# Performance work log

Measured on AMD Instinct MI355X. Metric: run time of the kernel, lower is better.

## Reference

```python
import jax, jax.numpy as jnp
import numpy as np

DIM = 2048
NH = 16
HD = 128
B = 32
BS = 16            # paged-KV block size
BLOCKS_PER_SEQ = 64
NUM_BLOCKS = B * BLOCKS_PER_SEQ
MAX_SEQ = BLOCKS_PER_SEQ * BS  # 1024
EPS = 1e-05


def _rms(x, w):
    return x * jax.lax.rsqrt(jnp.mean(x * x, axis=-1, keepdims=True) + EPS) * w


def setup_inputs() -> dict:
    key = jax.random.key(0)
    ks = jax.random.split(key, 12)
    init = lambda k, shape, fan: jax.random.normal(k, shape, jnp.float32) / np.float32(np.sqrt(fan))
    x = jax.random.normal(ks[0], (B, 1, DIM), jnp.float32)
    key_heap = jax.random.normal(ks[1], (NUM_BLOCKS, BS, NH, HD), jnp.float32)
    val_heap = jax.random.normal(ks[2], (NUM_BLOCKS, BS, NH, HD), jnp.float32)
    # each sequence owns a disjoint run of physical blocks
    block_table = jnp.arange(B * BLOCKS_PER_SEQ, dtype=jnp.int32).reshape(B, BLOCKS_PER_SEQ)
    context_lens = jax.random.randint(ks[3], (B,), 1, MAX_SEQ + 1, dtype=jnp.int32)
    last = context_lens - 1  # slot of the token being decoded
    blk = block_table[jnp.arange(B), last // BS]
    slot_mapping = (blk * BS + last % BS).astype(jnp.int32)
    return dict(
        x=x, key_heap=key_heap, val_heap=val_heap,
        wq=init(ks[4], (DIM, DIM), DIM), wk=init(ks[5], (DIM, DIM), DIM),
        wv=init(ks[6], (DIM, DIM), DIM), wo=init(ks[7], (DIM, DIM), DIM),
        w1=init(ks[8], (4 * DIM, DIM), DIM), w2=init(ks[9], (DIM, 4 * DIM), 4 * DIM),
        w3=init(ks[10], (4 * DIM, DIM), DIM),
        norm1_w=jnp.ones((DIM,), jnp.float32), norm2_w=jnp.ones((DIM,), jnp.float32),
        block_table=block_table, slot_mapping=slot_mapping,
        context_lens=context_lens, max_seq_len=MAX_SEQ,
    )


def reference(x, key_heap, val_heap, wq, wk, wv, wo, w1, w2, w3,
              norm1_w, norm2_w, block_table, slot_mapping, context_lens, max_seq_len):
    b = x.shape[0]
    nb, bs, H, D = key_heap.shape
    # --- Part 1: RMSNorm + QKV projections + paged cache write ---
    h = _rms(x, norm1_w)                       # [b,1,dim]
    q = (h @ wq.T).reshape(b, H, D)
    k = (h @ wk.T).reshape(b, H, D)
    v = (h @ wv.T).reshape(b, H, D)
    hk = key_heap.reshape(nb * bs, H, D).at[slot_mapping].set(k)
    hv = val_heap.reshape(nb * bs, H, D).at[slot_mapping].set(v)
    # --- Part 2: paged attention (gather blocks, masked softmax) ---
    keys = hk.reshape(nb, bs, H, D)[block_table].reshape(b, -1, H, D)  # [b,S,H,D]
    vals = hv.reshape(nb, bs, H, D)[block_table].reshape(b, -1, H, D)
    S = keys.shape[1]
    scale = np.float32(1.0 / np.sqrt(D))
    scores = jnp.einsum('bhd,bshd->bhs', q, keys) * scale
    mask = (jnp.arange(S)[None, :] < context_lens[:, None])[:, None, :]  # [b,1,S]
    probs = jax.nn.softmax(jnp.where(mask, scores, jnp.float32(-1e30)), axis=-1)
    attn = jnp.einsum('bhs,bshd->bhd', probs, vals).reshape(b, 1, H * D)
    # --- Part 3: output proj + residual + RMSNorm + SwiGLU MLP ---
    x = attn @ wo.T + x
    h2 = _rms(x, norm2_w)
    return (jax.nn.silu(h2 @ w1.T) * (h2 @ w3.T)) @ w2.T + x
```

## Files before the change

### kernel.cpp

```cpp
#include <hip/hip_runtime.h>
#include <math.h>

#define DIM 2048
#define NH 16
#define HD 128
#define NB 32
#define BS 16
#define BPS 64
#define KC 32

__global__ __launch_bounds__(256)
void rms_kernel(const float* __restrict__ in, const float* __restrict__ w,
                float* __restrict__ out)
{
    const int b = blockIdx.x;
    const int tid = threadIdx.x;
    const float* row = in + (size_t)b * DIM;
    const float4 a0 = *(const float4*)(row + tid * 8);
    const float4 a1 = *(const float4*)(row + tid * 8 + 4);
    float ss = a0.x*a0.x + a0.y*a0.y + a0.z*a0.z + a0.w*a0.w
             + a1.x*a1.x + a1.y*a1.y + a1.z*a1.z + a1.w*a1.w;
    ss += __shfl_xor(ss, 1);  ss += __shfl_xor(ss, 2);  ss += __shfl_xor(ss, 4);
    ss += __shfl_xor(ss, 8);  ss += __shfl_xor(ss, 16); ss += __shfl_xor(ss, 32);
    __shared__ float red[4];
    if ((tid & 63) == 0) red[tid >> 6] = ss;
    __syncthreads();
    const float mean = (red[0] + red[1] + red[2] + red[3]) * (1.0f / (float)DIM);
    const float r = rsqrtf(mean + 1e-5f);
    const float4 w0 = *(const float4*)(w + tid * 8);
    const float4 w1 = *(const float4*)(w + tid * 8 + 4);
    float4 o0, o1;
    o0.x = a0.x * r * w0.x; o0.y = a0.y * r * w0.y; o0.z = a0.z * r * w0.z; o0.w = a0.w * r * w0.w;
    o1.x = a1.x * r * w1.x; o1.y = a1.y * r * w1.y; o1.z = a1.z * r * w1.z; o1.w = a1.w * r * w1.w;
    *(float4*)(out + (size_t)b * DIM + tid * 8)     = o0;
    *(float4*)(out + (size_t)b * DIM + tid * 8 + 4) = o1;
}

__global__ __launch_bounds__(256)
void gemm_splitk(const float* __restrict__ W0, const float* __restrict__ W1,
                 const float* __restrict__ W2, int rows_per_w,
                 const float* __restrict__ act, int K, int Kblk,
                 float* __restrict__ partial, int M)
{
    __shared__ float Wt[KC][132];
    __shared__ float ht[KC][36];
    const int tid = threadIdx.x;
    const int m0 = blockIdx.x * 128;
    const int wi = m0 / rows_per_w;
    const float* __restrict__ W = (wi == 0) ? W0 : ((wi == 1) ? W1 : W2);
    const int row0 = m0 - wi * rows_per_w;
    const int k0b = blockIdx.y * Kblk;
    const int tr = tid & 31;
    const int tb = tid >> 5;
    const int sr = tid >> 3;
    const int skq = (tid & 7) * 4;

    float acc[4][4];
    #pragma unroll
    for (int i = 0; i < 4; i++) { acc[i][0]=0.f; acc[i][1]=0.f; acc[i][2]=0.f; acc[i][3]=0.f; }

    for (int k0 = k0b; k0 < k0b + Kblk; k0 += KC) {
        #pragma unroll
        for (int j = 0; j < 4; j++) {
            const int r = sr + j * 32;
            const float4 w4 = *(const float4*)(W + (size_t)(row0 + r) * K + k0 + skq);
            Wt[skq + 0][r] = w4.x; Wt[skq + 1][r] = w4.y;
            Wt[skq + 2][r] = w4.z; Wt[skq + 3][r] = w4.w;
        }
        {
            const float4 h4 = *(const float4*)(act + (size_t)sr * K + k0 + skq);
            ht[skq + 0][sr] = h4.x; ht[skq + 1][sr] = h4.y;
            ht[skq + 2][sr] = h4.z; ht[skq + 3][sr] = h4.w;
        }
        __syncthreads();
        #pragma unroll
        for (int k = 0; k < KC; k++) {
            const float4 w4 = *(const float4*)&Wt[k][tr * 4];
            const float4 h4 = *(const float4*)&ht[k][tb * 4];
            acc[0][0] += w4.x*h4.x; acc[0][1] += w4.x*h4.y; acc[0][2] += w4.x*h4.z; acc[0][3] += w4.x*h4.w;
            acc[1][0] += w4.y*h4.x; acc[1][1] += w4.y*h4.y; acc[1][2] += w4.y*h4.z; acc[1][3] += w4.y*h4.w;
            acc[2][0] += w4.z*h4.x; acc[2][1] += w4.z*h4.y; acc[2][2] += w4.z*h4.z; acc[2][3] += w4.z*h4.w;
            acc[3][0] += w4.w*h4.x; acc[3][1] += w4.w*h4.y; acc[3][2] += w4.w*h4.z; acc[3][3] += w4.w*h4.w;
        }
        __syncthreads();
    }
    #pragma unroll
    for (int i = 0; i < 4; i++) {
        const float4 o = make_float4(acc[i][0], acc[i][1], acc[i][2], acc[i][3]);
        *(float4*)(partial + ((size_t)blockIdx.y * M + m0 + tr * 4 + i) * 32 + tb * 4) = o;
    }
}

__global__ __launch_bounds__(256)
void reduce_qkv(const float* __restrict__ partial, float* __restrict__ q,
                float* __restrict__ kn, float* __restrict__ vn)
{
    const int e = blockIdx.x * 256 + threadIdx.x;
    const int m = e >> 5, b = e & 31;
    float s = 0.f;
    #pragma unroll
    for (int ks = 0; ks < 16; ks++) s += partial[((size_t)ks * 6144 + m) * 32 + b];
    if (m < 2048)      q [(size_t)b * DIM + m]        = s;
    else if (m < 4096) kn[(size_t)b * DIM + (m-2048)] = s;
    else               vn[(size_t)b * DIM + (m-4096)] = s;
}

__global__ __launch_bounds__(256)
void reduce_add(const float* __restrict__ partial, int KS, int M,
                const float* __restrict__ resid, float* __restrict__ out)
{
    const int e = blockIdx.x * 256 + threadIdx.x;
    const int m = e >> 5, b = e & 31;
    float s = 0.f;
    for (int ks = 0; ks < KS; ks++) s += partial[((size_t)ks * M + m) * 32 + b];
    out[(size_t)b * M + m] = s + resid[(size_t)b * M + m];
}

__global__ __launch_bounds__(256)
void reduce_m13(const float* __restrict__ partial, float* __restrict__ a)
{
    const int e = blockIdx.x * 256 + threadIdx.x;
    const int j = e >> 5, b = e & 31;
    float g = 0.f, u = 0.f;
    #pragma unroll
    for (int ks = 0; ks < 4; ks++) {
        g += partial[((size_t)ks * 16384 + j) * 32 + b];
        u += partial[((size_t)ks * 16384 + 8192 + j) * 32 + b];
    }
    const float sg = g / (1.0f + __expf(-g));
    a[(size_t)b * 8192 + j] = sg * u;
}

__global__ __launch_bounds__(256)
void attn_kernel(const float* __restrict__ q, const float* __restrict__ kn,
                 const float* __restrict__ vn, const float* __restrict__ key_heap,
                 const float* __restrict__ val_heap, const int* __restrict__ block_table,
                 const int* __restrict__ context_lens, float* __restrict__ attn_out)
{
    const int b  = blockIdx.x >> 4;
    const int hd = blockIdx.x & 15;
    const int tid  = threadIdx.x;
    const int wave = tid >> 6;
    const int lane = tid & 63;
    const int ps = lane >> 5;
    const int dl = lane & 31;
    const int ctxv = context_lens[b];

    __shared__ int   bt[BPS];
    __shared__ float sc[1024];
    __shared__ float red[8];
    __shared__ float wb[4][HD];

    if (tid < BPS) bt[tid] = block_table[b * BPS + tid];
    const float4 q4 = *(const float4*)(q + (size_t)b * DIM + hd * HD + dl * 4);
    __syncthreads();

    for (int s0 = wave * 2 + ps; s0 < ctxv; s0 += 8) {
        const float* kp = (s0 == ctxv - 1)
            ? (kn + (size_t)b * DIM + hd * HD)
            : (key_heap + ((size_t)(bt[s0 >> 4] * BS + (s0 & 15)) * NH + hd) * HD);
        const float4 k4 = *(const float4*)(kp + dl * 4);
        float d = q4.x*k4.x + q4.y*k4.y + q4.z*k4.z + q4.w*k4.w;
        d += __shfl_xor(d, 1); d += __shfl_xor(d, 2); d += __shfl_xor(d, 4);
        d += __shfl_xor(d, 8); d += __shfl_xor(d, 16);
        if (dl == 0) sc[s0] = d;
    }
    __syncthreads();

    float lm = -INFINITY;
    for (int i = tid; i < ctxv; i += 256) lm = fmaxf(lm, sc[i]);
    lm = fmaxf(lm, __shfl_xor(lm, 1));  lm = fmaxf(lm, __shfl_xor(lm, 2));
    lm = fmaxf(lm, __shfl_xor(lm, 4));  lm = fmaxf(lm, __shfl_xor(lm, 8));
    lm = fmaxf(lm, __shfl_xor(lm, 16)); lm = fmaxf(lm, __shfl_xor(lm, 32));
    if ((tid & 63) == 0) red[tid >> 6] = lm;
    __syncthreads();
    const float Mx = fmaxf(fmaxf(red[0], red[1]), fmaxf(red[2], red[3]));
    const float scale = 0.08838834764831845f;
    float lsum = 0.f;
    for (int i = tid; i < ctxv; i += 256) {
        const float p = __expf((sc[i] - Mx) * scale);
        sc[i] = p; lsum += p;
    }
    lsum += __shfl_xor(lsum, 1);  lsum += __shfl_xor(lsum, 2);  lsum += __shfl_xor(lsum, 4);
    lsum += __shfl_xor(lsum, 8);  lsum += __shfl_xor(lsum, 16); lsum += __shfl_xor(lsum, 32);
    if ((tid & 63) == 0) red[4 + (tid >> 6)] = lsum;
    __syncthreads();
    const float inv = 1.0f / (red[4] + red[5] + red[6] + red[7]);

    float4 acc = make_float4(0.f, 0.f, 0.f, 0.f);
    for (int s0 = wave * 2 + ps; s0 < ctxv; s0 += 8) {
        const float* vp = (s0 == ctxv - 1)
            ? (vn + (size_t)b * DIM + hd * HD)
            : (val_heap + ((size_t)(bt[s0 >> 4] * BS + (s0 & 15)) * NH + hd) * HD);
        const float4 v4 = *(const float4*)(vp + dl * 4);
        const float p = sc[s0];
        acc.x += p * v4.x; acc.y += p * v4.y; acc.z += p * v4.z; acc.w += p * v4.w;
    }
    acc.x += __shfl_xor(acc.x, 32); acc.y += __shfl_xor(acc.y, 32);
    acc.z += __shfl_xor(acc.z, 32); acc.w += __shfl_xor(acc.w, 32);
    if (lane < 32) *(float4*)&wb[wave][dl * 4] = acc;
    __syncthreads();
    if (tid < HD) {
        const float o = (wb[0][tid] + wb[1][tid] + wb[2][tid] + wb[3][tid]) * inv;
        attn_out[(size_t)b * DIM + hd * HD + tid] = o;
    }
}

extern "C" void kernel_launch(void* const* d_in, const int* in_sizes, int n_in,
                              void* d_out, int out_size, void* d_ws, size_t ws_size,
                              hipStream_t stream)
{
    const float* x        = (const float*)d_in[0];
    const float* key_heap = (const float*)d_in[1];
    const float* val_heap = (const float*)d_in[2];
    const float* wq = (const float*)d_in[3];
    const float* wk = (const float*)d_in[4];
    const float* wv = (const float*)d_in[5];
    const float* wo = (const float*)d_in[6];
    const float* w1 = (const float*)d_in[7];
    const float* w2 = (const float*)d_in[8];
    const float* w3 = (const float*)d_in[9];
    const float* n1w = (const float*)d_in[10];
    const float* n2w = (const float*)d_in[11];
    const int* btab = (const int*)d_in[12];
    const int* ctx  = (const int*)d_in[14];
    float* out = (float*)d_out;

    float* ws = (float*)d_ws;
    float* h1   = ws;
    float* qb   = ws + 65536;
    float* kn   = ws + 131072;
    float* vn   = ws + 196608;
    float* attn = ws + 262144;
    float* x2   = ws + 327680;
    float* h2   = ws + 393216;
    float* ab   = ws + 458752;
    float* pt   = ws + 720896;

    rms_kernel<<<32, 256, 0, stream>>>(x, n1w, h1);
    gemm_splitk<<<dim3(48, 16), 256, 0, stream>>>(wq, wk, wv, 2048, h1, 2048, 128, pt, 6144);
    reduce_qkv<<<768, 256, 0, stream>>>(pt, qb, kn, vn);
    attn_kernel<<<512, 256, 0, stream>>>(qb, kn, vn, key_heap, val_heap, btab, ctx, attn);
    gemm_splitk<<<dim3(16, 32), 256, 0, stream>>>(wo, wo, wo, 2048, attn, 2048, 64, pt, 2048);
    reduce_add<<<256, 256, 0, stream>>>(pt, 32, 2048, x, x2);
    rms_kernel<<<32, 256, 0, stream>>>(x2, n2w, h2);
    gemm_splitk<<<dim3(128, 4), 256, 0, stream>>>(w1, w3, w3, 8192, h2, 2048, 512, pt, 16384);
    reduce_m13<<<1024, 256, 0, stream>>>(pt, ab);
    gemm_splitk<<<dim3(16, 32), 256, 0, stream>>>(w2, w2, w2, 2048, ab, 8192, 256, pt, 2048);
    reduce_add<<<256, 256, 0, stream>>>(pt, 32, 2048, x2, out);
}
```

Baseline: 810.7 us.

## Split attention across sequence chunks and register-prefetch GEMM tiles

```diff
diff --git a/kernel.cpp b/kernel.cpp
--- a/kernel.cpp
+++ b/kernel.cpp
@@ -4,10 +4,11 @@
 #define DIM 2048
 #define NH 16
 #define HD 128
-#define NB 32
 #define BS 16
 #define BPS 64
 #define KC 32
+#define CS 128
+#define NSPLIT 8
 
 __global__ __launch_bounds__(256)
 void rms_kernel(const float* __restrict__ in, const float* __restrict__ w,
@@ -42,7 +43,7 @@
                  const float* __restrict__ act, int K, int Kblk,
                  float* __restrict__ partial, int M)
 {
-    __shared__ float Wt[KC][132];
+    __shared__ float Wt[KC][130];
     __shared__ float ht[KC][36];
     const int tid = threadIdx.x;
     const int m0 = blockIdx.x * 128;
@@ -50,44 +51,61 @@
     const float* __restrict__ W = (wi == 0) ? W0 : ((wi == 1) ? W1 : W2);
     const int row0 = m0 - wi * rows_per_w;
     const int k0b = blockIdx.y * Kblk;
-    const int tr = tid & 31;
-    const int tb = tid >> 5;
-    const int sr = tid >> 3;
+    const int tr2 = tid & 63;
+    const int tbg = tid >> 6;
+    const int sr  = tid >> 3;
     const int skq = (tid & 7) * 4;
 
-    float acc[4][4];
-    #pragma unroll
-    for (int i = 0; i < 4; i++) { acc[i][0]=0.f; acc[i][1]=0.f; acc[i][2]=0.f; acc[i][3]=0.f; }
-
-    for (int k0 = k0b; k0 < k0b + Kblk; k0 += KC) {
+    const int nchunk = Kblk / KC;
+    float4 wreg[4];
+    float4 hreg;
+    int k0 = k0b;
+    #pragma unroll
+    for (int j = 0; j < 4; j++)
+        wreg[j] = *(const float4*)(W + (size_t)(row0 + sr + j * 32) * K + k0 + skq);
+    hreg = *(const float4*)(act + (size_t)sr * K + k0 + skq);
+
+    float acc[2][8];
+    #pragma unroll
+    for (int i = 0; i < 2; i++)
+        #pragma unroll
+        for (int j = 0; j < 8; j++) acc[i][j] = 0.f;
+
+    for (int c = 0; c < nchunk; c++) {
         #pragma unroll
         for (int j = 0; j < 4; j++) {
             const int r = sr + j * 32;
-            const float4 w4 = *(const float4*)(W + (size_t)(row0 + r) * K + k0 + skq);
-            Wt[skq + 0][r] = w4.x; Wt[skq + 1][r] = w4.y;
-            Wt[skq + 2][r] = w4.z; Wt[skq + 3][r] = w4.w;
+            Wt[skq + 0][r] = wreg[j].x; Wt[skq + 1][r] = wreg[j].y;
+            Wt[skq + 2][r] = wreg[j].z; Wt[skq + 3][r] = wreg[j].w;
         }
-        {
-            const float4 h4 = *(const float4*)(act + (size_t)sr * K + k0 + skq);
-            ht[skq + 0][sr] = h4.x; ht[skq + 1][sr] = h4.y;
-            ht[skq + 2][sr] = h4.z; ht[skq + 3][sr] = h4.w;
+        ht[skq + 0][sr] = hreg.x; ht[skq + 1][sr] = hreg.y;
+        ht[skq + 2][sr] = hreg.z; ht[skq + 3][sr] = hreg.w;
+        __syncthreads();
+        if (c + 1 < nchunk) {
+            const int k1 = k0 + KC;
+            #pragma unroll
+            for (int j = 0; j < 4; j++)
+                wreg[j] = *(const float4*)(W + (size_t)(row0 + sr + j * 32) * K + k1 + skq);
+            hreg = *(const float4*)(act + (size_t)sr * K + k1 + skq);
+        }
+        #pragma unroll
+        for (int k = 0; k < KC; k++) {
+            const float2 w2v = *(const float2*)&Wt[k][tr2 * 2];
+            const float4 h0  = *(const float4*)&ht[k][tbg * 8];
+            const float4 h1  = *(const float4*)&ht[k][tbg * 8 + 4];
+            acc[0][0] += w2v.x*h0.x; acc[0][1] += w2v.x*h0.y; acc[0][2] += w2v.x*h0.z; acc[0][3] += w2v.x*h0.w;
+            acc[0][4] += w2v.x*h1.x; acc[0][5] += w2v.x*h1.y; acc[0][6] += w2v.x*h1.z; acc[0][7] += w2v.x*h1.w;
+            acc[1][0] += w2v.y*h0.x; acc[1][1] += w2v.y*h0.y; acc[1][2] += w2v.y*h0.z; acc[1][3] += w2v.y*h0.w;
+            acc[1][4] += w2v.y*h1.x; acc[1][5] += w2v.y*h1.y; acc[1][6] += w2v.y*h1.z; acc[1][7] += w2v.y*h1.w;
         }
         __syncthreads();
-        #pragma unroll
-        for (int k = 0; k < KC; k++) {
-            const float4 w4 = *(const float4*)&Wt[k][tr * 4];
-            const float4 h4 = *(const float4*)&ht[k][tb * 4];
-            acc[0][0] += w4.x*h4.x; acc[0][1] += w4.x*h4.y; acc[0][2] += w4.x*h4.z; acc[0][3] += w4.x*h4.w;
-            acc[1][0] += w4.y*h4.x; acc[1][1] += w4.y*h4.y; acc[1][2] += w4.y*h4.z; acc[1][3] += w4.y*h4.w;
-            acc[2][0] += w4.z*h4.x; acc[2][1] += w4.z*h4.y; acc[2][2] += w4.z*h4.z; acc[2][3] += w4.z*h4.w;
-            acc[3][0] += w4.w*h4.x; acc[3][1] += w4.w*h4.y; acc[3][2] += w4.w*h4.z; acc[3][3] += w4.w*h4.w;
-        }
-        __syncthreads();
-    }
-    #pragma unroll
-    for (int i = 0; i < 4; i++) {
-        const float4 o = make_float4(acc[i][0], acc[i][1], acc[i][2], acc[i][3]);
-        *(float4*)(partial + ((size_t)blockIdx.y * M + m0 + tr * 4 + i) * 32 + tb * 4) = o;
+        k0 += KC;
+    }
+    #pragma unroll
+    for (int i = 0; i < 2; i++) {
+        float* p = partial + ((size_t)blockIdx.y * M + m0 + tr2 * 2 + i) * 32 + tbg * 8;
+        *(float4*)p       = make_float4(acc[i][0], acc[i][1], acc[i][2], acc[i][3]);
+        *(float4*)(p + 4) = make_float4(acc[i][4], acc[i][5], acc[i][6], acc[i][7]);
     }
 }
 
@@ -132,43 +150,49 @@
 }
 
 __global__ __launch_bounds__(256)
-void attn_kernel(const float* __restrict__ q, const float* __restrict__ kn,
-                 const float* __restrict__ vn, const float* __restrict__ key_heap,
-                 const float* __restrict__ val_heap, const int* __restrict__ block_table,
-                 const int* __restrict__ context_lens, float* __restrict__ attn_out)
-{
-    const int b  = blockIdx.x >> 4;
-    const int hd = blockIdx.x & 15;
+void attn_split(const float* __restrict__ q, const float* __restrict__ kn,
+                const float* __restrict__ vn, const float* __restrict__ key_heap,
+                const float* __restrict__ val_heap, const int* __restrict__ block_table,
+                const int* __restrict__ context_lens,
+                float* __restrict__ pao, float* __restrict__ pml)
+{
+    const int split = blockIdx.x & 7;
+    const int hd    = (blockIdx.x >> 3) & 15;
+    const int b     = blockIdx.x >> 7;
+    const int ctxv  = context_lens[b];
+    const int s_begin = split * CS;
+    if (s_begin >= ctxv) return;
+    const int cnt = min(CS, ctxv - s_begin);
+
     const int tid  = threadIdx.x;
     const int wave = tid >> 6;
     const int lane = tid & 63;
     const int ps = lane >> 5;
     const int dl = lane & 31;
-    const int ctxv = context_lens[b];
-
-    __shared__ int   bt[BPS];
-    __shared__ float sc[1024];
+
+    __shared__ int   bt8[8];
+    __shared__ float sc[CS];
     __shared__ float red[8];
     __shared__ float wb[4][HD];
 
-    if (tid < BPS) bt[tid] = block_table[b * BPS + tid];
+    if (tid < 8) bt8[tid] = block_table[b * BPS + (s_begin >> 4) + tid];
     const float4 q4 = *(const float4*)(q + (size_t)b * DIM + hd * HD + dl * 4);
     __syncthreads();
 
-    for (int s0 = wave * 2 + ps; s0 < ctxv; s0 += 8) {
-        const float* kp = (s0 == ctxv - 1)
+    for (int i = wave * 2 + ps; i < cnt; i += 8) {
+        const int s = s_begin + i;
+        const float* kp = (s == ctxv - 1)
             ? (kn + (size_t)b * DIM + hd * HD)
-            : (key_heap + ((size_t)(bt[s0 >> 4] * BS + (s0 & 15)) * NH + hd) * HD);
+            : (key_heap + ((size_t)(bt8[i >> 4] * BS + (s & 15)) * NH + hd) * HD);
         const float4 k4 = *(const float4*)(kp + dl * 4);
         float d = q4.x*k4.x + q4.y*k4.y + q4.z*k4.z + q4.w*k4.w;
         d += __shfl_xor(d, 1); d += __shfl_xor(d, 2); d += __shfl_xor(d, 4);
         d += __shfl_xor(d, 8); d += __shfl_xor(d, 16);
-        if (dl == 0) sc[s0] = d;
-    }
-    __syncthreads();
-
-    float lm = -INFINITY;
-    for (int i = tid; i < ctxv; i += 256) lm = fmaxf(lm, sc[i]);
+        if (dl == 0) sc[i] = d;
+    }
+    __syncthreads();
+
+    float lm = (tid < cnt) ? sc[tid] : -INFINITY;
     lm = fmaxf(lm, __shfl_xor(lm, 1));  lm = fmaxf(lm, __shfl_xor(lm, 2));
     lm = fmaxf(lm, __shfl_xor(lm, 4));  lm = fmaxf(lm, __shfl_xor(lm, 8));
     lm = fmaxf(lm, __shfl_xor(lm, 16)); lm = fmaxf(lm, __shfl_xor(lm, 32));
@@ -177,23 +201,23 @@
     const float Mx = fmaxf(fmaxf(red[0], red[1]), fmaxf(red[2], red[3]));
     const float scale = 0.08838834764831845f;
     float lsum = 0.f;
-    for (int i = tid; i < ctxv; i += 256) {
-        const float p = __expf((sc[i] - Mx) * scale);
-        sc[i] = p; lsum += p;
+    if (tid < cnt) {
+        const float p = __expf((sc[tid] - Mx) * scale);
+        sc[tid] = p; lsum = p;
     }
     lsum += __shfl_xor(lsum, 1);  lsum += __shfl_xor(lsum, 2);  lsum += __shfl_xor(lsum, 4);
     lsum += __shfl_xor(lsum, 8);  lsum += __shfl_xor(lsum, 16); lsum += __shfl_xor(lsum, 32);
     if ((tid & 63) == 0) red[4 + (tid >> 6)] = lsum;
     __syncthreads();
-    const float inv = 1.0f / (red[4] + red[5] + red[6] + red[7]);
 
     float4 acc = make_float4(0.f, 0.f, 0.f, 0.f);
-    for (int s0 = wave * 2 + ps; s0 < ctxv; s0 += 8) {
-        const float* vp = (s0 == ctxv - 1)
+    for (int i = wave * 2 + ps; i < cnt; i += 8) {
+        const int s = s_begin + i;
+        const float* vp = (s == ctxv - 1)
             ? (vn + (size_t)b * DIM + hd * HD)
-            : (val_heap + ((size_t)(bt[s0 >> 4] * BS + (s0 & 15)) * NH + hd) * HD);
+            : (val_heap + ((size_t)(bt8[i >> 4] * BS + (s & 15)) * NH + hd) * HD);
         const float4 v4 = *(const float4*)(vp + dl * 4);
-        const float p = sc[s0];
+        const float p = sc[i];
         acc.x += p * v4.x; acc.y += p * v4.y; acc.z += p * v4.z; acc.w += p * v4.w;
     }
     acc.x += __shfl_xor(acc.x, 32); acc.y += __shfl_xor(acc.y, 32);
@@ -201,9 +225,37 @@
     if (lane < 32) *(float4*)&wb[wave][dl * 4] = acc;
     __syncthreads();
     if (tid < HD) {
-        const float o = (wb[0][tid] + wb[1][tid] + wb[2][tid] + wb[3][tid]) * inv;
-        attn_out[(size_t)b * DIM + hd * HD + tid] = o;
-    }
+        pao[(size_t)blockIdx.x * HD + tid] = wb[0][tid] + wb[1][tid] + wb[2][tid] + wb[3][tid];
+    }
+    if (tid == 0) {
+        pml[(size_t)blockIdx.x * 2]     = Mx;
+        pml[(size_t)blockIdx.x * 2 + 1] = red[4] + red[5] + red[6] + red[7];
+    }
+}
+
+__global__ __launch_bounds__(128)
+void attn_reduce(const float* __restrict__ pao, const float* __restrict__ pml,
+                 const int* __restrict__ context_lens, float* __restrict__ attn_out)
+{
+    const int bh = blockIdx.x;
+    const int b  = bh >> 4;
+    const int d  = threadIdx.x;
+    const int ns = (context_lens[b] + CS - 1) >> 7;
+    const float scale = 0.08838834764831845f;
+    float M = -INFINITY;
+    float ml[NSPLIT], ll[NSPLIT];
+    for (int s = 0; s < ns; s++) {
+        ml[s] = pml[((size_t)bh * NSPLIT + s) * 2];
+        ll[s] = pml[((size_t)bh * NSPLIT + s) * 2 + 1];
+        M = fmaxf(M, ml[s]);
+    }
+    float L = 0.f, o = 0.f;
+    for (int s = 0; s < ns; s++) {
+        const float f = __expf((ml[s] - M) * scale);
+        L += ll[s] * f;
+        o += pao[((size_t)bh * NSPLIT + s) * HD + d] * f;
+    }
+    attn_out[(size_t)bh * HD + d] = o / L;
 }
 
 extern "C" void kernel_launch(void* const* d_in, const int* in_sizes, int n_in,
@@ -236,11 +288,14 @@
     float* h2   = ws + 393216;
     float* ab   = ws + 458752;
     float* pt   = ws + 720896;
+    float* pao  = ws + 720896;
+    float* pml  = ws + 720896 + 524288;
 
     rms_kernel<<<32, 256, 0, stream>>>(x, n1w, h1);
     gemm_splitk<<<dim3(48, 16), 256, 0, stream>>>(wq, wk, wv, 2048, h1, 2048, 128, pt, 6144);
     reduce_qkv<<<768, 256, 0, stream>>>(pt, qb, kn, vn);
-    attn_kernel<<<512, 256, 0, stream>>>(qb, kn, vn, key_heap, val_heap, btab, ctx, attn);
+    attn_split<<<4096, 256, 0, stream>>>(qb, kn, vn, key_heap, val_heap, btab, ctx, pao, pml);
+    attn_reduce<<<512, 128, 0, stream>>>(pao, pml, ctx, attn);
     gemm_splitk<<<dim3(16, 32), 256, 0, stream>>>(wo, wo, wo, 2048, attn, 2048, 64, pt, 2048);
     reduce_add<<<256, 256, 0, stream>>>(pt, 32, 2048, x, x2);
     rms_kernel<<<32, 256, 0, stream>>>(x2, n2w, h2);
```

New measurement: 722.4 us. -10.9%, faster.
